# Optimization experiments

Hardware: AMD Instinct MI355X
Metric: run time of the kernel (lower is better)

Reference implementation:

```python
import jax, jax.numpy as jnp
import numpy as np

N_NODES = 50000
N_EDGES = 1000000
D_NODE = 64
D_EDGE = 64


def setup_inputs() -> dict:
    key = jax.random.key(0)
    ks = jax.random.split(key, 12)
    d, de = D_NODE, D_EDGE
    din = 2 * d + de
    s = lambda f_in: 1.0 / np.sqrt(f_in)
    return {
        "node_feat": jax.random.normal(ks[0], (N_NODES, d), jnp.float32),
        "edge_src": jax.random.randint(ks[1], (N_EDGES,), 0, N_NODES, jnp.int32),
        "edge_dst": jax.random.randint(ks[2], (N_EDGES,), 0, N_NODES, jnp.int32),
        "edge_feat": jax.random.normal(ks[3], (N_EDGES, de), jnp.float32),
        # msg_mlp: Linear(din,d) -> SiLU -> Linear(d,d)
        "W_m1": jax.random.uniform(ks[4], (din, d), jnp.float32, -s(din), s(din)),
        "b_m1": jax.random.uniform(ks[5], (d,), jnp.float32, -s(din), s(din)),
        "W_m2": jax.random.uniform(ks[6], (d, d), jnp.float32, -s(d), s(d)),
        "b_m2": jax.random.uniform(ks[7], (d,), jnp.float32, -s(d), s(d)),
        # update_mlp: Linear(d,d) -> SiLU -> Linear(d,d)
        "W_u1": jax.random.uniform(ks[8], (d, d), jnp.float32, -s(d), s(d)),
        "b_u1": jax.random.uniform(ks[9], (d,), jnp.float32, -s(d), s(d)),
        "W_u2": jax.random.uniform(ks[10], (d, d), jnp.float32, -s(d), s(d)),
        "b_u2": jax.random.uniform(ks[11], (d,), jnp.float32, -s(d), s(d)),
        # LayerNorm params
        "ln_gamma": jnp.ones((d,), jnp.float32),
        "ln_beta": jnp.zeros((d,), jnp.float32),
    }


def _layer_norm(x, gamma, beta, eps=1e-5):
    mu = jnp.mean(x, axis=-1, keepdims=True)
    var = jnp.var(x, axis=-1, keepdims=True)
    return (x - mu) * jax.lax.rsqrt(var + eps) * gamma + beta


def reference(node_feat, edge_src, edge_dst, edge_feat,
              W_m1, b_m1, W_m2, b_m2, W_u1, b_u1, W_u2, b_u2,
              ln_gamma, ln_beta):
    # gather endpoint features per edge: [E, 2d+de]
    msg_input = jnp.concatenate(
        [node_feat[edge_src], node_feat[edge_dst], edge_feat], axis=-1)
    h = jax.nn.silu(msg_input @ W_m1 + b_m1)
    messages = h @ W_m2 + b_m2                      # [E, d]
    aggregated = jax.ops.segment_sum(messages, edge_dst,
                                     num_segments=node_feat.shape[0])
    upd = jax.nn.silu(aggregated @ W_u1 + b_u1) @ W_u2 + b_u2
    return _layer_norm(node_feat + upd, ln_gamma, ln_beta)
```

## Files before the change

kernel.cpp:

```cpp
#include <hip/hip_runtime.h>
#include <stdint.h>

typedef __bf16 bf16;
typedef __attribute__((ext_vector_type(8))) bf16 bf16x8;
typedef __attribute__((ext_vector_type(4))) float f32x4;

#define D 64
#define EPW 32

__device__ __forceinline__ float silu_f(float x) {
    return x / (1.0f + __expf(-x));
}

__global__ void hist_kernel(const int* __restrict__ edst, int* __restrict__ cnt, int E) {
    const int stride = gridDim.x * blockDim.x;
    for (int e = blockIdx.x * blockDim.x + threadIdx.x; e < E; e += stride)
        atomicAdd(&cnt[edst[e]], 1);
}

__global__ void scan_part_kernel(const int* __restrict__ cnt, int* __restrict__ part, int N) {
    __shared__ int red[256];
    const int t = threadIdx.x, idx = blockIdx.x * 256 + t;
    red[t] = (idx < N) ? cnt[idx] : 0;
    __syncthreads();
    for (int off = 128; off; off >>= 1) {
        if (t < off) red[t] += red[t + off];
        __syncthreads();
    }
    if (t == 0) part[blockIdx.x] = red[0];
}

__global__ void scan_base_kernel(int* __restrict__ part, int nblk) {
    __shared__ int sc[256];
    const int t = threadIdx.x;
    const int v = (t < nblk) ? part[t] : 0;
    sc[t] = v;
    __syncthreads();
    for (int off = 1; off < 256; off <<= 1) {
        int u = (t >= off) ? sc[t - off] : 0;
        __syncthreads();
        sc[t] += u;
        __syncthreads();
    }
    part[t] = sc[t] - v;
}

__global__ void scan_fin_kernel(const int* __restrict__ cnt, const int* __restrict__ part,
                                int* __restrict__ cur, int N) {
    __shared__ int sc[256];
    const int t = threadIdx.x, idx = blockIdx.x * 256 + t;
    const int v = (idx < N) ? cnt[idx] : 0;
    sc[t] = v;
    __syncthreads();
    for (int off = 1; off < 256; off <<= 1) {
        int u = (t >= off) ? sc[t - off] : 0;
        __syncthreads();
        sc[t] += u;
        __syncthreads();
    }
    if (idx < N) cur[idx] = sc[t] - v + part[blockIdx.x];
}

__global__ void scatter_kernel(const int* __restrict__ edst, int* __restrict__ cur,
                               int* __restrict__ spos, int E) {
    const int stride = gridDim.x * blockDim.x;
    for (int e = blockIdx.x * blockDim.x + threadIdx.x; e < E; e += stride) {
        int pos = atomicAdd(&cur[edst[e]], 1);
        spos[e] = pos;
    }
}

__global__ void cvt_nf_kernel(const float* __restrict__ nf, bf16* __restrict__ nfb, int total8) {
    const int i = blockIdx.x * blockDim.x + threadIdx.x;
    if (i < total8) {
        f32x4 a = ((const f32x4*)nf)[i*2], b = ((const f32x4*)nf)[i*2 + 1];
        bf16x8 v;
        #pragma unroll
        for (int k = 0; k < 4; ++k) { v[k] = (bf16)a[k]; v[4+k] = (bf16)b[k]; }
        ((bf16x8*)nfb)[i] = v;
    }
}

__launch_bounds__(256, 3)
__global__ void mp_edge_kernel(
    const float* __restrict__ node_feat,
    const bf16*  __restrict__ nfb,
    const int*   __restrict__ esrc,
    const int*   __restrict__ edst,
    const float* __restrict__ efeat,
    const int*   __restrict__ spos,
    const float* __restrict__ W1, const float* __restrict__ b1,
    const float* __restrict__ W2, const float* __restrict__ b2,
    bf16* __restrict__ msgbuf,
    float* __restrict__ agg,
    int E)
{
    __shared__ __align__(16) bf16 W1f[6*4*64*8];
    __shared__ __align__(16) bf16 W2f[2*4*64*8];
    __shared__ __align__(16) bf16 HM[4][32*72];
    __shared__ float b1s[D], b2s[D];

    const int t    = threadIdx.x;
    const int lane = t & 63;
    const int w    = t >> 6;
    const int g    = lane >> 4;
    const int c    = lane & 15;

    for (int idx = t; idx < 6*4*64; idx += 256) {
        int l = idx & 63, nt = (idx >> 6) & 3, ks = idx >> 8;
        int k0 = ks*32 + (l >> 4)*8, col = nt*16 + (l & 15);
        bf16x8 v;
        #pragma unroll
        for (int i = 0; i < 8; ++i) v[i] = (bf16)W1[(k0 + i)*D + col];
        *(bf16x8*)&W1f[idx*8] = v;
    }
    for (int idx = t; idx < 2*4*64; idx += 256) {
        int l = idx & 63, nt = (idx >> 6) & 3, ks = idx >> 8;
        int k0 = ks*32 + (l >> 4)*8, col = nt*16 + (l & 15);
        bf16x8 v;
        #pragma unroll
        for (int i = 0; i < 8; ++i) v[i] = (bf16)W2[(k0 + i)*D + col];
        *(bf16x8*)&W2f[idx*8] = v;
    }
    if (t < D) { b1s[t] = b1[t]; b2s[t] = b2[t]; }
    __syncthreads();

    bf16* hm = &HM[w][0];
    const int nwt = (E + EPW - 1) / EPW;
    const int t0  = blockIdx.x*4 + w;
    const int tstride = gridDim.x*4;

    int nse0=0, nde0=0, nsp0=0, nse1=0, nde1=0, nsp1=0;
    if (t0 < nwt) {
        const int q0 = min(t0*EPW + c, E - 1);
        const int q1 = min(t0*EPW + 16 + c, E - 1);
        nse0 = esrc[q0]; nde0 = edst[q0];
        nse1 = esrc[q1]; nde1 = edst[q1];
        if (spos) { nsp0 = spos[q0]; nsp1 = spos[q1]; }
    }

    for (int tile = t0; tile < nwt; tile += tstride) {
        const int e0 = tile * EPW;
        const int se0 = nse0, de0 = nde0, sp0 = nsp0;
        const int se1 = nse1, de1 = nde1, sp1 = nsp1;
        const int tn = tile + tstride;
        if (tn < nwt) {
            const int q0 = min(tn*EPW + c, E - 1);
            const int q1 = min(tn*EPW + 16 + c, E - 1);
            nse0 = esrc[q0]; nde0 = edst[q0];
            nse1 = esrc[q1]; nde1 = edst[q1];
            if (spos) { nsp0 = spos[q0]; nsp1 = spos[q1]; }
        }
        const int r0 = min(e0 + c,      E - 1);
        const int r1 = min(e0 + 16 + c, E - 1);

        bf16x8 an[8];
        f32x4  ef[8];
        if (nfb) {
            #pragma unroll
            for (int ks = 0; ks < 4; ++ks) {
                const int row0 = (ks < 2) ? se0 : de0;
                const int row1 = (ks < 2) ? se1 : de1;
                const int coff = (ks & 1)*32 + g*8;
                an[ks*2]   = *(const bf16x8*)&nfb[(size_t)row0*D + coff];
                an[ks*2+1] = *(const bf16x8*)&nfb[(size_t)row1*D + coff];
            }
        } else {
            #pragma unroll
            for (int ks = 0; ks < 4; ++ks) {
                const int row0 = (ks < 2) ? se0 : de0;
                const int row1 = (ks < 2) ? se1 : de1;
                const int coff = (ks & 1)*32 + g*8;
                const float* p0 = node_feat + (size_t)row0*D + coff;
                const float* p1 = node_feat + (size_t)row1*D + coff;
                f32x4 xa = ((const f32x4*)p0)[0], xb = ((const f32x4*)p0)[1];
                f32x4 ya = ((const f32x4*)p1)[0], yb = ((const f32x4*)p1)[1];
                bf16x8 a0, a1;
                #pragma unroll
                for (int i = 0; i < 4; ++i) {
                    a0[i] = (bf16)xa[i];  a0[4+i] = (bf16)xb[i];
                    a1[i] = (bf16)ya[i];  a1[4+i] = (bf16)yb[i];
                }
                an[ks*2] = a0; an[ks*2+1] = a1;
            }
        }
        #pragma unroll
        for (int ks2 = 0; ks2 < 2; ++ks2) {
            const int coff = ks2*32 + g*8;
            const float* p0 = efeat + (size_t)r0*D + coff;
            const float* p1 = efeat + (size_t)r1*D + coff;
            ef[ks2*4+0] = ((const f32x4*)p0)[0];
            ef[ks2*4+1] = ((const f32x4*)p0)[1];
            ef[ks2*4+2] = ((const f32x4*)p1)[0];
            ef[ks2*4+3] = ((const f32x4*)p1)[1];
        }

        f32x4 acc0[4] = {f32x4{0,0,0,0}, f32x4{0,0,0,0}, f32x4{0,0,0,0}, f32x4{0,0,0,0}};
        f32x4 acc1[4] = {f32x4{0,0,0,0}, f32x4{0,0,0,0}, f32x4{0,0,0,0}, f32x4{0,0,0,0}};
        #pragma unroll
        for (int ks = 0; ks < 4; ++ks) {
            #pragma unroll
            for (int n = 0; n < 4; ++n) {
                bf16x8 bb = *(const bf16x8*)&W1f[((ks*4 + n)*64 + lane)*8];
                acc0[n] = __builtin_amdgcn_mfma_f32_16x16x32_bf16(an[ks*2],   bb, acc0[n], 0, 0, 0);
                acc1[n] = __builtin_amdgcn_mfma_f32_16x16x32_bf16(an[ks*2+1], bb, acc1[n], 0, 0, 0);
            }
        }
        #pragma unroll
        for (int ks2 = 0; ks2 < 2; ++ks2) {
            bf16x8 a0, a1;
            #pragma unroll
            for (int i = 0; i < 4; ++i) {
                a0[i]   = (bf16)ef[ks2*4+0][i];
                a0[4+i] = (bf16)ef[ks2*4+1][i];
                a1[i]   = (bf16)ef[ks2*4+2][i];
                a1[4+i] = (bf16)ef[ks2*4+3][i];
            }
            #pragma unroll
            for (int n = 0; n < 4; ++n) {
                bf16x8 bb = *(const bf16x8*)&W1f[(((ks2+4)*4 + n)*64 + lane)*8];
                acc0[n] = __builtin_amdgcn_mfma_f32_16x16x32_bf16(a0, bb, acc0[n], 0, 0, 0);
                acc1[n] = __builtin_amdgcn_mfma_f32_16x16x32_bf16(a1, bb, acc1[n], 0, 0, 0);
            }
        }

        #pragma unroll
        for (int n = 0; n < 4; ++n) {
            const int col = n*16 + c;
            const float bias = b1s[col];
            #pragma unroll
            for (int j = 0; j < 4; ++j) {
                hm[(g*4 + j)*72 + col]      = (bf16)silu_f(acc0[n][j] + bias);
                hm[(16 + g*4 + j)*72 + col] = (bf16)silu_f(acc1[n][j] + bias);
            }
        }

        f32x4 acc2a[4] = {f32x4{0,0,0,0}, f32x4{0,0,0,0}, f32x4{0,0,0,0}, f32x4{0,0,0,0}};
        f32x4 acc2b[4] = {f32x4{0,0,0,0}, f32x4{0,0,0,0}, f32x4{0,0,0,0}, f32x4{0,0,0,0}};
        #pragma unroll
        for (int ks = 0; ks < 2; ++ks) {
            bf16x8 a0 = *(const bf16x8*)&hm[c*72        + ks*32 + g*8];
            bf16x8 a1 = *(const bf16x8*)&hm[(16 + c)*72 + ks*32 + g*8];
            #pragma unroll
            for (int n = 0; n < 4; ++n) {
                bf16x8 bb = *(const bf16x8*)&W2f[((ks*4 + n)*64 + lane)*8];
                acc2a[n] = __builtin_amdgcn_mfma_f32_16x16x32_bf16(a0, bb, acc2a[n], 0, 0, 0);
                acc2b[n] = __builtin_amdgcn_mfma_f32_16x16x32_bf16(a1, bb, acc2b[n], 0, 0, 0);
            }
        }

        if (msgbuf) {
            asm volatile("s_waitcnt lgkmcnt(0)" ::: "memory");
            #pragma unroll
            for (int n = 0; n < 4; ++n) {
                const int col = n*16 + c;
                const float bias = b2s[col];
                #pragma unroll
                for (int j = 0; j < 4; ++j) {
                    hm[(g*4 + j)*72 + col]      = (bf16)(acc2a[n][j] + bias);
                    hm[(16 + g*4 + j)*72 + col] = (bf16)(acc2b[n][j] + bias);
                }
            }
            #pragma unroll
            for (int it = 0; it < 4; ++it) {
                const int row   = (lane >> 3) + it*8;
                const int chunk = lane & 7;
                const int sp = (it < 2) ? __shfl(sp0, row) : __shfl(sp1, row - 16);
                if (e0 + row < E)
                    *(bf16x8*)&msgbuf[(size_t)sp*64 + chunk*8] =
                        *(const bf16x8*)&hm[row*72 + chunk*8];
            }
        } else {
            #pragma unroll
            for (int j = 0; j < 4; ++j) {
                const int row = g*4 + j;
                const int d0 = __shfl(de0, row);
                const int d1 = __shfl(de1, row);
                const bool ok0 = (e0 + row)      < E;
                const bool ok1 = (e0 + 16 + row) < E;
                #pragma unroll
                for (int n = 0; n < 4; ++n) {
                    const int col = n*16 + c;
                    if (ok0) atomicAdd(&agg[(size_t)d0*D + col], acc2a[n][j] + b2s[col]);
                    if (ok1) atomicAdd(&agg[(size_t)d1*D + col], acc2b[n][j] + b2s[col]);
                }
            }
        }
    }
}

__launch_bounds__(256, 8)
__global__ void agg_kernel(const bf16* __restrict__ msgbuf,
                           const int* __restrict__ cnt,
                           const int* __restrict__ cur,
                           float* __restrict__ agg,
                           int N)
{
    const int lane = threadIdx.x & 63;
    const int w    = threadIdx.x >> 6;
    const int p    = lane >> 3;
    const int cb   = lane & 7;
    for (int n = blockIdx.x*4 + w; n < N; n += gridDim.x*4) {
        const int end = cur[n];
        const int beg = end - cnt[n];
        float s[8] = {0,0,0,0,0,0,0,0};
        for (int i = beg + p; i < end; i += 8) {
            bf16x8 v = *(const bf16x8*)&msgbuf[(size_t)i*64 + cb*8];
            #pragma unroll
            for (int k = 0; k < 8; ++k) s[k] += (float)v[k];
        }
        #pragma unroll
        for (int off = 8; off < 64; off <<= 1) {
            #pragma unroll
            for (int k = 0; k < 8; ++k) s[k] += __shfl_xor(s[k], off);
        }
        if (lane < 8) {
            f32x4 lo = {s[0], s[1], s[2], s[3]};
            f32x4 hi = {s[4], s[5], s[6], s[7]};
            *(f32x4*)&agg[(size_t)n*D + lane*8]     = lo;
            *(f32x4*)&agg[(size_t)n*D + lane*8 + 4] = hi;
        }
    }
}

__launch_bounds__(256, 4)
__global__ void node_gemm_kernel(
    const float* __restrict__ node_feat,
    const float* __restrict__ Wu1, const float* __restrict__ bu1,
    const float* __restrict__ Wu2, const float* __restrict__ bu2,
    const float* __restrict__ gamma, const float* __restrict__ beta,
    float* __restrict__ inout, int N)
{
    __shared__ __align__(16) bf16 Wf1[2*4*64*8];
    __shared__ __align__(16) bf16 Wf2[2*4*64*8];
    __shared__ __align__(16) bf16 Hs[4][16*72];
    __shared__ float b1s[D], b2s[D], gs[D], bs[D];

    const int t    = threadIdx.x;
    const int lane = t & 63;
    const int w    = t >> 6;
    const int g    = lane >> 4;
    const int c    = lane & 15;

    for (int idx = t; idx < 2*4*64; idx += 256) {
        int l = idx & 63, nt = (idx >> 6) & 3, ks = idx >> 8;
        int k0 = ks*32 + (l >> 4)*8, col = nt*16 + (l & 15);
        bf16x8 v1, v2;
        #pragma unroll
        for (int i = 0; i < 8; ++i) {
            v1[i] = (bf16)Wu1[(k0 + i)*D + col];
            v2[i] = (bf16)Wu2[(k0 + i)*D + col];
        }
        *(bf16x8*)&Wf1[idx*8] = v1;
        *(bf16x8*)&Wf2[idx*8] = v2;
    }
    if (t < D) { b1s[t] = bu1[t]; b2s[t] = bu2[t]; gs[t] = gamma[t]; bs[t] = beta[t]; }
    __syncthreads();

    const int base = blockIdx.x*64 + w*16;
    if (base >= N) return;
    bf16* hs = &Hs[w][0];

    f32x4 acc[4] = {f32x4{0,0,0,0}, f32x4{0,0,0,0}, f32x4{0,0,0,0}, f32x4{0,0,0,0}};
    #pragma unroll
    for (int ks = 0; ks < 2; ++ks) {
        const int rowA = min(base + c, N - 1);
        const float* p = inout + (size_t)rowA*D + ks*32 + g*8;
        f32x4 xa = ((const f32x4*)p)[0], xb = ((const f32x4*)p)[1];
        bf16x8 a;
        #pragma unroll
        for (int i = 0; i < 4; ++i) { a[i] = (bf16)xa[i]; a[4+i] = (bf16)xb[i]; }
        #pragma unroll
        for (int n = 0; n < 4; ++n) {
            bf16x8 bb = *(const bf16x8*)&Wf1[((ks*4 + n)*64 + lane)*8];
            acc[n] = __builtin_amdgcn_mfma_f32_16x16x32_bf16(a, bb, acc[n], 0, 0, 0);
        }
    }
    #pragma unroll
    for (int n = 0; n < 4; ++n) {
        const int col = n*16 + c;
        const float bias = b1s[col];
        #pragma unroll
        for (int j = 0; j < 4; ++j)
            hs[(g*4 + j)*72 + col] = (bf16)silu_f(acc[n][j] + bias);
    }

    f32x4 acc2[4] = {f32x4{0,0,0,0}, f32x4{0,0,0,0}, f32x4{0,0,0,0}, f32x4{0,0,0,0}};
    #pragma unroll
    for (int ks = 0; ks < 2; ++ks) {
        bf16x8 a = *(const bf16x8*)&hs[c*72 + ks*32 + g*8];
        #pragma unroll
        for (int n = 0; n < 4; ++n) {
            bf16x8 bb = *(const bf16x8*)&Wf2[((ks*4 + n)*64 + lane)*8];
            acc2[n] = __builtin_amdgcn_mfma_f32_16x16x32_bf16(a, bb, acc2[n], 0, 0, 0);
        }
    }

    float y[4][4];
    #pragma unroll
    for (int n = 0; n < 4; ++n) {
        const int col = n*16 + c;
        #pragma unroll
        for (int j = 0; j < 4; ++j) {
            const int row = base + g*4 + j;
            const float x0 = (row < N) ? node_feat[(size_t)row*D + col] : 0.f;
            y[n][j] = x0 + acc2[n][j] + b2s[col];
        }
    }
    #pragma unroll
    for (int j = 0; j < 4; ++j) {
        float s1 = 0.f, s2 = 0.f;
        #pragma unroll
        for (int n = 0; n < 4; ++n) { s1 += y[n][j]; s2 += y[n][j]*y[n][j]; }
        #pragma unroll
        for (int m = 1; m < 16; m <<= 1) {
            s1 += __shfl_xor(s1, m);
            s2 += __shfl_xor(s2, m);
        }
        const float mu  = s1 * (1.0f/64.0f);
        const float var = s2 * (1.0f/64.0f) - mu*mu;
        const float rs  = rsqrtf(var + 1e-5f);
        const int row = base + g*4 + j;
        if (row < N) {
            #pragma unroll
            for (int n = 0; n < 4; ++n) {
                const int col = n*16 + c;
                inout[(size_t)row*D + col] = (y[n][j] - mu)*rs*gs[col] + bs[col];
            }
        }
    }
}

extern "C" void kernel_launch(void* const* d_in, const int* in_sizes, int n_in,
                              void* d_out, int out_size, void* d_ws, size_t ws_size,
                              hipStream_t stream) {
    const float* node_feat = (const float*)d_in[0];
    const int*   esrc      = (const int*)d_in[1];
    const int*   edst      = (const int*)d_in[2];
    const float* efeat     = (const float*)d_in[3];
    const float* W_m1      = (const float*)d_in[4];
    const float* b_m1      = (const float*)d_in[5];
    const float* W_m2      = (const float*)d_in[6];
    const float* b_m2      = (const float*)d_in[7];
    const float* W_u1      = (const float*)d_in[8];
    const float* b_u1      = (const float*)d_in[9];
    const float* W_u2      = (const float*)d_in[10];
    const float* b_u2      = (const float*)d_in[11];
    const float* ln_gamma  = (const float*)d_in[12];
    const float* ln_beta   = (const float*)d_in[13];

    float* out = (float*)d_out;
    const int E = in_sizes[1];
    const int N = in_sizes[0] / D;

    const size_t msg_bytes = (((size_t)E * D * 2) + 255) & ~(size_t)255;
    const size_t int_bytes = ((sizeof(int) * ((size_t)E + 2*(size_t)N + 256)) + 255) & ~(size_t)255;
    const size_t nfb_bytes = (((size_t)N * D * 2) + 255) & ~(size_t)255;
    const size_t need_csr  = msg_bytes + int_bytes;
    const size_t need_full = need_csr + nfb_bytes;

    const int nwt   = (E + EPW - 1) / EPW;
    const int nblk  = (nwt + 3) / 4;
    const int grid1 = nblk < 768 ? nblk : 768;
    const int gridN = (N + 63) / 64;
    const int nchunk = (N + 255) / 256;

    const bool csr     = ws_size >= need_csr;
    const bool use_nfb = ws_size >= (csr ? need_full : nfb_bytes);

    bf16* msgbuf = nullptr;
    int  *spos = nullptr, *cnt = nullptr, *cur = nullptr, *part = nullptr;
    bf16* nfb = nullptr;

    if (csr) {
        msgbuf = (bf16*)d_ws;
        spos   = (int*)((char*)d_ws + msg_bytes);
        cnt    = spos + E;
        cur    = cnt + N;
        part   = cur + N;
        if (use_nfb) nfb = (bf16*)((char*)d_ws + need_csr);
    } else if (use_nfb) {
        nfb = (bf16*)d_ws;
    }

    if (use_nfb) {
        const int total8 = N * D / 8;
        cvt_nf_kernel<<<(total8 + 255)/256, 256, 0, stream>>>(node_feat, nfb, total8);
    }

    if (csr) {
        hipMemsetAsync(cnt, 0, sizeof(int)*(size_t)N, stream);
        hist_kernel     <<<1024, 256, 0, stream>>>(edst, cnt, E);
        scan_part_kernel<<<nchunk, 256, 0, stream>>>(cnt, part, N);
        scan_base_kernel<<<1, 256, 0, stream>>>(part, nchunk);
        scan_fin_kernel <<<nchunk, 256, 0, stream>>>(cnt, part, cur, N);
        scatter_kernel  <<<1024, 256, 0, stream>>>(edst, cur, spos, E);

        mp_edge_kernel<<<grid1, 256, 0, stream>>>(node_feat, nfb, esrc, edst, efeat, spos,
                                                  W_m1, b_m1, W_m2, b_m2,
                                                  msgbuf, nullptr, E);
        agg_kernel<<<2048, 256, 0, stream>>>(msgbuf, cnt, cur, out, N);
    } else {
        hipMemsetAsync(out, 0, (size_t)N * D * sizeof(float), stream);
        mp_edge_kernel<<<grid1, 256, 0, stream>>>(node_feat, nfb, esrc, edst, efeat, nullptr,
                                                  W_m1, b_m1, W_m2, b_m2,
                                                  nullptr, out, E);
    }

    node_gemm_kernel<<<gridN, 256, 0, stream>>>(node_feat, W_u1, b_u1, W_u2, b_u2,
                                                ln_gamma, ln_beta, out, N);
}
```

Before: 249.3 us.

## Pre-sort edges by destination and reduce segments in-tile instead of message buffer

Adds a permute kernel that writes edge features as bf16 and (src,dst) pairs in destination-sorted order. The edge kernel then reads sorted edges, reduces runs of equal destinations inside each 32-edge tile, and writes interior segments directly while using atomics only at tile boundaries. This removes the separate bf16 message buffer and aggregation kernel. The cost is an extra pass that reads all fp32 edge features and scatter-writes them, plus a memset of the output.

```diff
diff --git a/kernel.cpp b/kernel.cpp
--- a/kernel.cpp
+++ b/kernel.cpp
@@ -81,17 +81,43 @@
     }
 }
 
+__global__ void permute_kernel(const int* __restrict__ esrc,
+                               const int* __restrict__ edst,
+                               const float* __restrict__ efeat,
+                               const int* __restrict__ spos,
+                               int2* __restrict__ sd,
+                               bf16* __restrict__ efb,
+                               int E)
+{
+    const int gw   = (blockIdx.x * blockDim.x + threadIdx.x) >> 6;
+    const int nw   = (gridDim.x * blockDim.x) >> 6;
+    const int lane = threadIdx.x & 63;
+    const int sub  = lane >> 3, ch = lane & 7;
+
+    for (int base = gw * 8; base < E; base += nw * 8) {
+        const int e = base + sub;
+        const bool v = e < E;
+        const int ee = v ? e : E - 1;
+        const int sp = spos[ee];
+        const float* p = efeat + (size_t)ee * D + ch * 8;
+        f32x4 x = ((const f32x4*)p)[0], y = ((const f32x4*)p)[1];
+        bf16x8 o;
+        #pragma unroll
+        for (int i = 0; i < 4; ++i) { o[i] = (bf16)x[i]; o[4+i] = (bf16)y[i]; }
+        if (v) {
+            *(bf16x8*)&efb[(size_t)sp * D + ch * 8] = o;
+            if (ch == 0) sd[sp] = make_int2(esrc[ee], edst[ee]);
+        }
+    }
+}
+
 __launch_bounds__(256, 3)
-__global__ void mp_edge_kernel(
-    const float* __restrict__ node_feat,
-    const bf16*  __restrict__ nfb,
-    const int*   __restrict__ esrc,
-    const int*   __restrict__ edst,
-    const float* __restrict__ efeat,
-    const int*   __restrict__ spos,
+__global__ void mp_edge_sorted_kernel(
+    const bf16* __restrict__ nfb,
+    const int2* __restrict__ sd,
+    const bf16* __restrict__ efb,
     const float* __restrict__ W1, const float* __restrict__ b1,
     const float* __restrict__ W2, const float* __restrict__ b2,
-    bf16* __restrict__ msgbuf,
     float* __restrict__ agg,
     int E)
 {
@@ -127,72 +153,30 @@
 
     bf16* hm = &HM[w][0];
     const int nwt = (E + EPW - 1) / EPW;
-    const int t0  = blockIdx.x*4 + w;
-    const int tstride = gridDim.x*4;
-
-    int nse0=0, nde0=0, nsp0=0, nse1=0, nde1=0, nsp1=0;
-    if (t0 < nwt) {
-        const int q0 = min(t0*EPW + c, E - 1);
-        const int q1 = min(t0*EPW + 16 + c, E - 1);
-        nse0 = esrc[q0]; nde0 = edst[q0];
-        nse1 = esrc[q1]; nde1 = edst[q1];
-        if (spos) { nsp0 = spos[q0]; nsp1 = spos[q1]; }
-    }
-
-    for (int tile = t0; tile < nwt; tile += tstride) {
+
+    for (int tile = blockIdx.x*4 + w; tile < nwt; tile += gridDim.x*4) {
         const int e0 = tile * EPW;
-        const int se0 = nse0, de0 = nde0, sp0 = nsp0;
-        const int se1 = nse1, de1 = nde1, sp1 = nsp1;
-        const int tn = tile + tstride;
-        if (tn < nwt) {
-            const int q0 = min(tn*EPW + c, E - 1);
-            const int q1 = min(tn*EPW + 16 + c, E - 1);
-            nse0 = esrc[q0]; nde0 = edst[q0];
-            nse1 = esrc[q1]; nde1 = edst[q1];
-            if (spos) { nsp0 = spos[q0]; nsp1 = spos[q1]; }
-        }
         const int r0 = min(e0 + c,      E - 1);
         const int r1 = min(e0 + 16 + c, E - 1);
-
-        bf16x8 an[8];
-        f32x4  ef[8];
-        if (nfb) {
-            #pragma unroll
-            for (int ks = 0; ks < 4; ++ks) {
-                const int row0 = (ks < 2) ? se0 : de0;
-                const int row1 = (ks < 2) ? se1 : de1;
-                const int coff = (ks & 1)*32 + g*8;
-                an[ks*2]   = *(const bf16x8*)&nfb[(size_t)row0*D + coff];
-                an[ks*2+1] = *(const bf16x8*)&nfb[(size_t)row1*D + coff];
-            }
-        } else {
-            #pragma unroll
-            for (int ks = 0; ks < 4; ++ks) {
-                const int row0 = (ks < 2) ? se0 : de0;
-                const int row1 = (ks < 2) ? se1 : de1;
-                const int coff = (ks & 1)*32 + g*8;
-                const float* p0 = node_feat + (size_t)row0*D + coff;
-                const float* p1 = node_feat + (size_t)row1*D + coff;
-                f32x4 xa = ((const f32x4*)p0)[0], xb = ((const f32x4*)p0)[1];
-                f32x4 ya = ((const f32x4*)p1)[0], yb = ((const f32x4*)p1)[1];
-                bf16x8 a0, a1;
-                #pragma unroll
-                for (int i = 0; i < 4; ++i) {
-                    a0[i] = (bf16)xa[i];  a0[4+i] = (bf16)xb[i];
-                    a1[i] = (bf16)ya[i];  a1[4+i] = (bf16)yb[i];
-                }
-                an[ks*2] = a0; an[ks*2+1] = a1;
-            }
+        const int2 p0 = sd[r0];
+        const int2 p1 = sd[r1];
+        const int se0 = p0.x, de0 = p0.y;
+        const int se1 = p1.x, de1 = p1.y;
+
+        bf16x8 an[8], ae[4];
+        #pragma unroll
+        for (int ks = 0; ks < 4; ++ks) {
+            const int row0 = (ks < 2) ? se0 : de0;
+            const int row1 = (ks < 2) ? se1 : de1;
+            const int coff = (ks & 1)*32 + g*8;
+            an[ks*2]   = *(const bf16x8*)&nfb[(size_t)row0*D + coff];
+            an[ks*2+1] = *(const bf16x8*)&nfb[(size_t)row1*D + coff];
         }
         #pragma unroll
         for (int ks2 = 0; ks2 < 2; ++ks2) {
             const int coff = ks2*32 + g*8;
-            const float* p0 = efeat + (size_t)r0*D + coff;
-            const float* p1 = efeat + (size_t)r1*D + coff;
-            ef[ks2*4+0] = ((const f32x4*)p0)[0];
-            ef[ks2*4+1] = ((const f32x4*)p0)[1];
-            ef[ks2*4+2] = ((const f32x4*)p1)[0];
-            ef[ks2*4+3] = ((const f32x4*)p1)[1];
+            ae[ks2*2]   = *(const bf16x8*)&efb[(size_t)r0*D + coff];
+            ae[ks2*2+1] = *(const bf16x8*)&efb[(size_t)r1*D + coff];
         }
 
         f32x4 acc0[4] = {f32x4{0,0,0,0}, f32x4{0,0,0,0}, f32x4{0,0,0,0}, f32x4{0,0,0,0}};
@@ -208,19 +192,11 @@
         }
         #pragma unroll
         for (int ks2 = 0; ks2 < 2; ++ks2) {
-            bf16x8 a0, a1;
-            #pragma unroll
-            for (int i = 0; i < 4; ++i) {
-                a0[i]   = (bf16)ef[ks2*4+0][i];
-                a0[4+i] = (bf16)ef[ks2*4+1][i];
-                a1[i]   = (bf16)ef[ks2*4+2][i];
-                a1[4+i] = (bf16)ef[ks2*4+3][i];
-            }
             #pragma unroll
             for (int n = 0; n < 4; ++n) {
                 bf16x8 bb = *(const bf16x8*)&W1f[(((ks2+4)*4 + n)*64 + lane)*8];
-                acc0[n] = __builtin_amdgcn_mfma_f32_16x16x32_bf16(a0, bb, acc0[n], 0, 0, 0);
-                acc1[n] = __builtin_amdgcn_mfma_f32_16x16x32_bf16(a1, bb, acc1[n], 0, 0, 0);
+                acc0[n] = __builtin_amdgcn_mfma_f32_16x16x32_bf16(ae[ks2*2],   bb, acc0[n], 0, 0, 0);
+                acc1[n] = __builtin_amdgcn_mfma_f32_16x16x32_bf16(ae[ks2*2+1], bb, acc1[n], 0, 0, 0);
             }
         }
 
@@ -249,76 +225,157 @@
             }
         }
 
-        if (msgbuf) {
-            asm volatile("s_waitcnt lgkmcnt(0)" ::: "memory");
+        asm volatile("s_waitcnt lgkmcnt(0)" ::: "memory");
+
+        #pragma unroll
+        for (int n = 0; n < 4; ++n) {
+            const int col = n*16 + c;
+            const float bias = b2s[col];
+            #pragma unroll
+            for (int j = 0; j < 4; ++j) {
+                hm[(g*4 + j)*72 + col]      = (bf16)(acc2a[n][j] + bias);
+                hm[(16 + g*4 + j)*72 + col] = (bf16)(acc2b[n][j] + bias);
+            }
+        }
+
+        const int da = __shfl(de0, lane & 15);
+        const int db = __shfl(de1, lane & 15);
+        const int row = lane & 31;
+        int rowd = (lane & 16) ? db : da;
+        if (e0 + row >= E) rowd = -1;
+        const int prevd = __shfl(rowd, (lane + 63) & 63);
+        const bool st = (row == 0) || (rowd != prevd);
+        unsigned long long m = __ballot(st) & 0xFFFFFFFFull;
+
+        while (m) {
+            const int a = __builtin_ctzll(m); m &= m - 1;
+            const int rb = m ? __builtin_ctzll(m) : 32;
+            const int d = __shfl(rowd, a);
+            if (d >= 0) {
+                float s = 0.f;
+                for (int r = a; r < rb; ++r) s += (float)hm[r*72 + lane];
+                float* dp = &agg[(size_t)d*D + lane];
+                if (a > 0 && rb < 32) *dp = s;
+                else atomicAdd(dp, s);
+            }
+        }
+    }
+}
+
+__launch_bounds__(256, 3)
+__global__ void mp_edge_atomic_kernel(
+    const float* __restrict__ node_feat,
+    const int*   __restrict__ esrc,
+    const int*   __restrict__ edst,
+    const float* __restrict__ efeat,
+    const float* __restrict__ W1, const float* __restrict__ b1,
+    const float* __restrict__ W2, const float* __restrict__ b2,
+    float* __restrict__ agg,
+    int E)
+{
+    __shared__ __align__(16) bf16 W1f[6*4*64*8];
+    __shared__ __align__(16) bf16 W2f[2*4*64*8];
+    __shared__ __align__(16) bf16 HM[4][32*72];
+    __shared__ float b1s[D], b2s[D];
+
+    const int t    = threadIdx.x;
+    const int lane = t & 63;
+    const int w    = t >> 6;
+    const int g    = lane >> 4;
+    const int c    = lane & 15;
+
+    for (int idx = t; idx < 6*4*64; idx += 256) {
+        int l = idx & 63, nt = (idx >> 6) & 3, ks = idx >> 8;
+        int k0 = ks*32 + (l >> 4)*8, col = nt*16 + (l & 15);
+        bf16x8 v;
+        #pragma unroll
+        for (int i = 0; i < 8; ++i) v[i] = (bf16)W1[(k0 + i)*D + col];
+        *(bf16x8*)&W1f[idx*8] = v;
+    }
+    for (int idx = t; idx < 2*4*64; idx += 256) {
+        int l = idx & 63, nt = (idx >> 6) & 3, ks = idx >> 8;
+        int k0 = ks*32 + (l >> 4)*8, col = nt*16 + (l & 15);
+        bf16x8 v;
+        #pragma unroll
+        for (int i = 0; i < 8; ++i) v[i] = (bf16)W2[(k0 + i)*D + col];
+        *(bf16x8*)&W2f[idx*8] = v;
+    }
+    if (t < D) { b1s[t] = b1[t]; b2s[t] = b2[t]; }
+    __syncthreads();
+
+    bf16* hm = &HM[w][0];
+    const int nwt = (E + EPW - 1) / EPW;
+
+    for (int tile = blockIdx.x*4 + w; tile < nwt; tile += gridDim.x*4) {
+        const int e0 = tile * EPW;
+        const int r0 = min(e0 + c,      E - 1);
+        const int r1 = min(e0 + 16 + c, E - 1);
+        const int se0 = esrc[r0], de0 = edst[r0];
+        const int se1 = esrc[r1], de1 = edst[r1];
+
+        f32x4 acc0[4] = {f32x4{0,0,0,0}, f32x4{0,0,0,0}, f32x4{0,0,0,0}, f32x4{0,0,0,0}};
+        f32x4 acc1[4] = {f32x4{0,0,0,0}, f32x4{0,0,0,0}, f32x4{0,0,0,0}, f32x4{0,0,0,0}};
+        #pragma unroll
+        for (int ks = 0; ks < 6; ++ks) {
+            const int col = ks*32 + g*8;
+            const float *p0, *p1;
+            if (col < 64)       { p0 = node_feat + (size_t)se0*D + col;        p1 = node_feat + (size_t)se1*D + col; }
+            else if (col < 128) { p0 = node_feat + (size_t)de0*D + (col - 64); p1 = node_feat + (size_t)de1*D + (col - 64); }
+            else                { p0 = efeat + (size_t)r0*D + (col - 128);     p1 = efeat + (size_t)r1*D + (col - 128); }
+            f32x4 xa = ((const f32x4*)p0)[0], xb = ((const f32x4*)p0)[1];
+            f32x4 ya = ((const f32x4*)p1)[0], yb = ((const f32x4*)p1)[1];
+            bf16x8 a0, a1;
+            #pragma unroll
+            for (int i = 0; i < 4; ++i) {
+                a0[i] = (bf16)xa[i];  a0[4+i] = (bf16)xb[i];
+                a1[i] = (bf16)ya[i];  a1[4+i] = (bf16)yb[i];
+            }
+            #pragma unroll
+            for (int n = 0; n < 4; ++n) {
+                bf16x8 bb = *(const bf16x8*)&W1f[((ks*4 + n)*64 + lane)*8];
+                acc0[n] = __builtin_amdgcn_mfma_f32_16x16x32_bf16(a0, bb, acc0[n], 0, 0, 0);
+                acc1[n] = __builtin_amdgcn_mfma_f32_16x16x32_bf16(a1, bb, acc1[n], 0, 0, 0);
+            }
+        }
+
+        #pragma unroll
+        for (int n = 0; n < 4; ++n) {
+            const int col = n*16 + c;
+            const float bias = b1s[col];
+            #pragma unroll
+            for (int j = 0; j < 4; ++j) {
+                hm[(g*4 + j)*72 + col]      = (bf16)silu_f(acc0[n][j] + bias);
+                hm[(16 + g*4 + j)*72 + col] = (bf16)silu_f(acc1[n][j] + bias);
+            }
+        }
+
+        f32x4 acc2a[4] = {f32x4{0,0,0,0}, f32x4{0,0,0,0}, f32x4{0,0,0,0}, f32x4{0,0,0,0}};
+        f32x4 acc2b[4] = {f32x4{0,0,0,0}, f32x4{0,0,0,0}, f32x4{0,0,0,0}, f32x4{0,0,0,0}};
+        #pragma unroll
+        for (int ks = 0; ks < 2; ++ks) {
+            bf16x8 a0 = *(const bf16x8*)&hm[c*72        + ks*32 + g*8];
+            bf16x8 a1 = *(const bf16x8*)&hm[(16 + c)*72 + ks*32 + g*8];
+            #pragma unroll
+            for (int n = 0; n < 4; ++n) {
+                bf16x8 bb = *(const bf16x8*)&W2f[((ks*4 + n)*64 + lane)*8];
+                acc2a[n] = __builtin_amdgcn_mfma_f32_16x16x32_bf16(a0, bb, acc2a[n], 0, 0, 0);
+                acc2b[n] = __builtin_amdgcn_mfma_f32_16x16x32_bf16(a1, bb, acc2b[n], 0, 0, 0);
+            }
+        }
+
+        #pragma unroll
+        for (int j = 0; j < 4; ++j) {
+            const int row = g*4 + j;
+            const int d0 = __shfl(de0, row);
+            const int d1 = __shfl(de1, row);
+            const bool ok0 = (e0 + row)      < E;
+            const bool ok1 = (e0 + 16 + row) < E;
             #pragma unroll
             for (int n = 0; n < 4; ++n) {
                 const int col = n*16 + c;
-                const float bias = b2s[col];
-                #pragma unroll
-                for (int j = 0; j < 4; ++j) {
-                    hm[(g*4 + j)*72 + col]      = (bf16)(acc2a[n][j] + bias);
-                    hm[(16 + g*4 + j)*72 + col] = (bf16)(acc2b[n][j] + bias);
-                }
-            }
-            #pragma unroll
-            for (int it = 0; it < 4; ++it) {
-                const int row   = (lane >> 3) + it*8;
-                const int chunk = lane & 7;
-                const int sp = (it < 2) ? __shfl(sp0, row) : __shfl(sp1, row - 16);
-                if (e0 + row < E)
-                    *(bf16x8*)&msgbuf[(size_t)sp*64 + chunk*8] =
-                        *(const bf16x8*)&hm[row*72 + chunk*8];
-            }
-        } else {
-            #pragma unroll
-            for (int j = 0; j < 4; ++j) {
-                const int row = g*4 + j;
-                const int d0 = __shfl(de0, row);
-                const int d1 = __shfl(de1, row);
-                const bool ok0 = (e0 + row)      < E;
-                const bool ok1 = (e0 + 16 + row) < E;
-                #pragma unroll
-                for (int n = 0; n < 4; ++n) {
-                    const int col = n*16 + c;
-                    if (ok0) atomicAdd(&agg[(size_t)d0*D + col], acc2a[n][j] + b2s[col]);
-                    if (ok1) atomicAdd(&agg[(size_t)d1*D + col], acc2b[n][j] + b2s[col]);
-                }
-            }
-        }
-    }
-}
-
-__launch_bounds__(256, 8)
-__global__ void agg_kernel(const bf16* __restrict__ msgbuf,
-                           const int* __restrict__ cnt,
-                           const int* __restrict__ cur,
-                           float* __restrict__ agg,
-                           int N)
-{
-    const int lane = threadIdx.x & 63;
-    const int w    = threadIdx.x >> 6;
-    const int p    = lane >> 3;
-    const int cb   = lane & 7;
-    for (int n = blockIdx.x*4 + w; n < N; n += gridDim.x*4) {
-        const int end = cur[n];
-        const int beg = end - cnt[n];
-        float s[8] = {0,0,0,0,0,0,0,0};
-        for (int i = beg + p; i < end; i += 8) {
-            bf16x8 v = *(const bf16x8*)&msgbuf[(size_t)i*64 + cb*8];
-            #pragma unroll
-            for (int k = 0; k < 8; ++k) s[k] += (float)v[k];
-        }
-        #pragma unroll
-        for (int off = 8; off < 64; off <<= 1) {
-            #pragma unroll
-            for (int k = 0; k < 8; ++k) s[k] += __shfl_xor(s[k], off);
-        }
-        if (lane < 8) {
-            f32x4 lo = {s[0], s[1], s[2], s[3]};
-            f32x4 hi = {s[4], s[5], s[6], s[7]};
-            *(f32x4*)&agg[(size_t)n*D + lane*8]     = lo;
-            *(f32x4*)&agg[(size_t)n*D + lane*8 + 4] = hi;
+                if (ok0) atomicAdd(&agg[(size_t)d0*D + col], acc2a[n][j] + b2s[col]);
+                if (ok1) atomicAdd(&agg[(size_t)d1*D + col], acc2b[n][j] + b2s[col]);
+            }
         }
     }
 }
@@ -413,9 +470,9 @@
         #pragma unroll
         for (int n = 0; n < 4; ++n) { s1 += y[n][j]; s2 += y[n][j]*y[n][j]; }
         #pragma unroll
-        for (int m = 1; m < 16; m <<= 1) {
-            s1 += __shfl_xor(s1, m);
-            s2 += __shfl_xor(s2, m);
+        for (int mm = 1; mm < 16; mm <<= 1) {
+            s1 += __shfl_xor(s1, mm);
+            s2 += __shfl_xor(s2, mm);
         }
         const float mu  = s1 * (1.0f/64.0f);
         const float var = s2 * (1.0f/64.0f) - mu*mu;
@@ -453,11 +510,11 @@
     const int E = in_sizes[1];
     const int N = in_sizes[0] / D;
 
-    const size_t msg_bytes = (((size_t)E * D * 2) + 255) & ~(size_t)255;
+    const size_t efb_bytes = (((size_t)E * D * 2) + 255) & ~(size_t)255;
+    const size_t sd_bytes  = (((size_t)E * 8) + 255) & ~(size_t)255;
     const size_t int_bytes = ((sizeof(int) * ((size_t)E + 2*(size_t)N + 256)) + 255) & ~(size_t)255;
     const size_t nfb_bytes = (((size_t)N * D * 2) + 255) & ~(size_t)255;
-    const size_t need_csr  = msg_bytes + int_bytes;
-    const size_t need_full = need_csr + nfb_bytes;
+    const size_t need = efb_bytes + sd_bytes + int_bytes + nfb_bytes;
 
     const int nwt   = (E + EPW - 1) / EPW;
     const int nblk  = (nwt + 3) / 4;
@@ -465,30 +522,18 @@
     const int gridN = (N + 63) / 64;
     const int nchunk = (N + 255) / 256;
 
-    const bool csr     = ws_size >= need_csr;
-    const bool use_nfb = ws_size >= (csr ? need_full : nfb_bytes);
-
-    bf16* msgbuf = nullptr;
-    int  *spos = nullptr, *cnt = nullptr, *cur = nullptr, *part = nullptr;
-    bf16* nfb = nullptr;
-
-    if (csr) {
-        msgbuf = (bf16*)d_ws;
-        spos   = (int*)((char*)d_ws + msg_bytes);
-        cnt    = spos + E;
-        cur    = cnt + N;
-        part   = cur + N;
-        if (use_nfb) nfb = (bf16*)((char*)d_ws + need_csr);
-    } else if (use_nfb) {
-        nfb = (bf16*)d_ws;
-    }
-
-    if (use_nfb) {
+    if (ws_size >= need) {
+        bf16* efb  = (bf16*)d_ws;
+        int2* sd   = (int2*)((char*)d_ws + efb_bytes);
+        int*  spos = (int*)((char*)d_ws + efb_bytes + sd_bytes);
+        int*  cnt  = spos + E;
+        int*  cur  = cnt + N;
+        int*  part = cur + N;
+        bf16* nfb  = (bf16*)((char*)d_ws + efb_bytes + sd_bytes + int_bytes);
+
         const int total8 = N * D / 8;
         cvt_nf_kernel<<<(total8 + 255)/256, 256, 0, stream>>>(node_feat, nfb, total8);
-    }
-
-    if (csr) {
+
         hipMemsetAsync(cnt, 0, sizeof(int)*(size_t)N, stream);
         hist_kernel     <<<1024, 256, 0, stream>>>(edst, cnt, E);
         scan_part_kernel<<<nchunk, 256, 0, stream>>>(cnt, part, N);
@@ -496,15 +541,17 @@
         scan_fin_kernel <<<nchunk, 256, 0, stream>>>(cnt, part, cur, N);
         scatter_kernel  <<<1024, 256, 0, stream>>>(edst, cur, spos, E);
 
-        mp_edge_kernel<<<grid1, 256, 0, stream>>>(node_feat, nfb, esrc, edst, efeat, spos,
-                                                  W_m1, b_m1, W_m2, b_m2,
-                                                  msgbuf, nullptr, E);
-        agg_kernel<<<2048, 256, 0, stream>>>(msgbuf, cnt, cur, out, N);
+        permute_kernel<<<2048, 256, 0, stream>>>(esrc, edst, efeat, spos, sd, efb, E);
+
+        hipMemsetAsync(out, 0, (size_t)N * D * sizeof(float), stream);
+        mp_edge_sorted_kernel<<<grid1, 256, 0, stream>>>(nfb, sd, efb,
+                                                         W_m1, b_m1, W_m2, b_m2,
+                                                         out, E);
     } else {
         hipMemsetAsync(out, 0, (size_t)N * D * sizeof(float), stream);
-        mp_edge_kernel<<<grid1, 256, 0, stream>>>(node_feat, nfb, esrc, edst, efeat, nullptr,
-                                                  W_m1, b_m1, W_m2, b_m2,
-                                                  nullptr, out, E);
+        mp_edge_atomic_kernel<<<grid1, 256, 0, stream>>>(node_feat, esrc, edst, efeat,
+                                                         W_m1, b_m1, W_m2, b_m2,
+                                                         out, E);
     }
 
     node_gemm_kernel<<<gridN, 256, 0, stream>>>(node_feat, W_u1, b_u1, W_u2, b_u2,
```

Result: slower. 290.7 us (+16.6%).
